# Performance work log

Measured on AMD Instinct MI355X. Metric: run time of the kernel, lower is better.

The kernel has to match this reference:

```python
import jax, jax.numpy as jnp
import numpy as np

K = 20
EPS = 1e-5


def _knn(x, k):
    # x: [B, C, N] -> indices of k nearest points, [B, N, k]
    sq = jnp.sum(x * x, axis=1)  # [B, N]
    neg_d2 = 2.0 * jnp.einsum('bcn,bcm->bnm', x, x) - sq[:, None, :] - sq[:, :, None]
    return jax.lax.top_k(neg_d2, k)[1]


def _graph_feature(x, idx):
    # x: [B, C, N], idx: [B, N, k] -> edge features [B, 2C, N, k]
    xT = x.transpose(0, 2, 1)  # [B, N, C]
    nbr = jax.vmap(lambda t, i: t[i])(xT, idx)  # [B, N, k, C]
    ctr = jnp.broadcast_to(xT[:, :, None, :], nbr.shape)
    f = jnp.concatenate([nbr - ctr, ctr], axis=-1)  # [B, N, k, 2C]
    return f.transpose(0, 3, 1, 2)


def _lrelu(x):
    return jnp.where(x > 0, x, 0.2 * x)


def _bn(x, g, b):
    # eval-mode BatchNorm with freshly-initialized running stats (mean=0, var=1)
    shp = (1, -1) + (1,) * (x.ndim - 2)
    return x * (g / jnp.sqrt(1.0 + EPS)).reshape(shp) + b.reshape(shp)


def _c2(x, w):  # 1x1 Conv2d, no bias
    return jnp.einsum('oi,bink->bonk', w, x)


def _c1(x, w):  # 1x1 Conv1d, no bias
    return jnp.einsum('oi,bin->bon', w, x)


def reference(coords, feats, w1, w2, w3, w4, w5, w6, w7, w8, w9,
              g15, b15, g6, b6, g7, b7, g8, b8):
    x0 = jnp.concatenate([coords.transpose(0, 2, 1), feats], axis=1)  # [B, 6, N]
    n = x0.shape[2]
    # EdgeConv block 1 (kNN on xyz only)
    x = _graph_feature(x0, _knn(x0[:, :3], K))  # [B, 12, N, k]
    x = _lrelu(_bn(_c2(x, w1), g15[0], b15[0]))
    x = _lrelu(_bn(_c2(x, w2), g15[1], b15[1]))
    x1 = jnp.max(x, axis=-1)  # [B, 64, N]
    # EdgeConv block 2 (dynamic kNN in feature space)
    x = _graph_feature(x1, _knn(x1, K))
    x = _lrelu(_bn(_c2(x, w3), g15[2], b15[2]))
    x = _lrelu(_bn(_c2(x, w4), g15[3], b15[3]))
    x2 = jnp.max(x, axis=-1)
    # EdgeConv block 3
    x = _graph_feature(x2, _knn(x2, K))
    x3 = jnp.max(_lrelu(_bn(_c2(x, w5), g15[4], b15[4])), axis=-1)
    # global embedding + per-point head
    xc = jnp.concatenate([x1, x2, x3], axis=1)  # [B, 192, N]
    x = _lrelu(_bn(_c1(xc, w6), g6, b6))  # [B, 1024, N]
    gmax = jnp.max(x, axis=-1, keepdims=True)
    x = jnp.concatenate([jnp.broadcast_to(gmax, (x.shape[0], x.shape[1], n)), x1, x2, x3], axis=1)  # [B,1216,N]
    x = _lrelu(_bn(_c1(x, w7), g7, b7))
    x = _lrelu(_bn(_c1(x, w8), g8, b8))
    # dropout is identity in eval mode
    x = _c1(x, w9)  # [B, 20, N]
    return x.transpose(0, 2, 1).reshape(-1, w9.shape[0])


def setup_inputs() -> dict:
    key = jax.random.key(0)
    ks = jax.random.split(key, 16)
    B, N, C = 8, 4096, 3
    s = 0.1
    return {
        'coords': jax.random.uniform(ks[0], (B, N, 3), jnp.float32),
        'feats': jax.random.normal(ks[1], (B, C, N), jnp.float32),
        'w1': s * jax.random.normal(ks[2], (64, 12), jnp.float32),
        'w2': s * jax.random.normal(ks[3], (64, 64), jnp.float32),
        'w3': s * jax.random.normal(ks[4], (64, 128), jnp.float32),
        'w4': s * jax.random.normal(ks[5], (64, 64), jnp.float32),
        'w5': s * jax.random.normal(ks[6], (64, 128), jnp.float32),
        'w6': s * jax.random.normal(ks[7], (1024, 192), jnp.float32),
        'w7': s * jax.random.normal(ks[8], (512, 1216), jnp.float32),
        'w8': s * jax.random.normal(ks[9], (256, 512), jnp.float32),
        'w9': s * jax.random.normal(ks[10], (20, 256), jnp.float32),
        'g15': jnp.ones((5, 64), jnp.float32),
        'b15': jnp.zeros((5, 64), jnp.float32),
        'g6': jnp.ones((1024,), jnp.float32),
        'b6': jnp.zeros((1024,), jnp.float32),
        'g7': jnp.ones((512,), jnp.float32),
        'b7': jnp.zeros((512,), jnp.float32),
        'g8': jnp.ones((256,), jnp.float32),
        'b8': jnp.zeros((256,), jnp.float32),
    }
```

## Files before the change

### kernel.cpp

```cpp
#include <hip/hip_runtime.h>
#include <math.h>

#define BB 8
#define NN 4096
#define KNN 20
#define EPSBN 1e-5f

__device__ __forceinline__ float lrelu(float x){ return x > 0.f ? x : 0.2f*x; }
__device__ __forceinline__ unsigned encf(float f){
  unsigned u = __float_as_uint(f);
  return (u & 0x80000000u) ? ~u : (u | 0x80000000u);
}
__device__ __forceinline__ float decf(unsigned u){
  return (u & 0x80000000u) ? __uint_as_float(u & 0x7fffffffu) : __uint_as_float(~u);
}
__device__ __forceinline__ float rdlane(float v, int l){
  return __uint_as_float(__builtin_amdgcn_readlane(__float_as_uint(v), l));
}

__global__ void prep_w(float* __restrict__ dst, const float* __restrict__ src,
                       int O, int I, int ld, int coff, const float* __restrict__ g){
  int tot = O*I;
  for(int t = blockIdx.x*blockDim.x + threadIdx.x; t < tot; t += gridDim.x*blockDim.x){
    int o = t % O, i = t / O;
    float s = g ? g[o] * (1.0f/sqrtf(1.0f+EPSBN)) : 1.0f;
    dst[(size_t)i*O + o] = src[(size_t)o*ld + coff + i] * s;
  }
}

__global__ void init_gmax(unsigned* __restrict__ g){
  int t = blockIdx.x*blockDim.x + threadIdx.x;
  if(t < BB*1024) g[t] = 0u;
}

__global__ void build_x0(const float* __restrict__ coords, const float* __restrict__ feats,
                         float* __restrict__ x0p){
  int p = blockIdx.x*blockDim.x + threadIdx.x;
  if(p >= BB*NN) return;
  int b = p / NN, n = p % NN;
  x0p[(size_t)p*6+0] = coords[(size_t)p*3+0];
  x0p[(size_t)p*6+1] = coords[(size_t)p*3+1];
  x0p[(size_t)p*6+2] = coords[(size_t)p*3+2];
  #pragma unroll
  for(int cc=0; cc<3; ++cc) x0p[(size_t)p*6+3+cc] = feats[((size_t)b*3+cc)*NN + n];
}

template<int D, int LD>
__global__ __launch_bounds__(256,3) void knn_kernel(const float* __restrict__ X, int coloff,
                                                    int* __restrict__ idxOut){
  constexpr int IG = 4;
  __shared__ float stage[2][IG][256];
  __shared__ float xi_s[IG][(D+3)&~3];
  __shared__ float sqi_s[IG];
  const int t = threadIdx.x;
  const int w = t >> 6, l = t & 63;
  const int b = blockIdx.x / (NN/IG);
  const int i0 = (blockIdx.x % (NN/IG)) * IG;
  const float* Xb = X + (size_t)b*NN*LD + coloff;

  for(int u = t; u < IG*D; u += 256) xi_s[u/D][u%D] = Xb[(size_t)(i0 + u/D)*LD + (u%D)];
  __syncthreads();
  if(t < IG){
    float s = 0.f;
    for(int d=0; d<D; ++d){ float v = xi_s[t][d]; s = fmaf(v, v, s); }
    sqi_s[t] = s;
  }
  __syncthreads();

  float v1=-INFINITY, v2=-INFINITY, v3=-INFINITY;
  int   j1=0x7fffffff, j2=0x7fffffff, j3=0x7fffffff;

  auto ins = [&](float v, int jj){
    bool b1 = v > v1, b2 = v > v2, b3 = v > v3;
    v3 = b3 ? (b2 ? v2 : v) : v3;
    j3 = b3 ? (b2 ? j2 : jj) : j3;
    v2 = b2 ? (b1 ? v1 : v) : v2;
    j2 = b2 ? (b1 ? j1 : jj) : j2;
    v1 = b1 ? v : v1;
    j1 = b1 ? jj : j1;
  };

  for(int s = 0; s < NN/256; ++s){
    const int j = s*256 + t;
    const float* row = Xb + (size_t)j*LD;
    float dot0=0.f,dot1=0.f,dot2=0.f,dot3=0.f,sqj=0.f;
    if constexpr (D % 4 == 0){
      #pragma unroll
      for(int d0=0; d0<D; d0+=4){
        const float4 v = *reinterpret_cast<const float4*>(row + d0);
        sqj = fmaf(v.x,v.x,sqj); sqj = fmaf(v.y,v.y,sqj);
        sqj = fmaf(v.z,v.z,sqj); sqj = fmaf(v.w,v.w,sqj);
        const float4 w0 = *reinterpret_cast<const float4*>(&xi_s[0][d0]);
        const float4 w1 = *reinterpret_cast<const float4*>(&xi_s[1][d0]);
        const float4 w2 = *reinterpret_cast<const float4*>(&xi_s[2][d0]);
        const float4 w3 = *reinterpret_cast<const float4*>(&xi_s[3][d0]);
        dot0 = fmaf(v.x,w0.x,dot0); dot0 = fmaf(v.y,w0.y,dot0);
        dot0 = fmaf(v.z,w0.z,dot0); dot0 = fmaf(v.w,w0.w,dot0);
        dot1 = fmaf(v.x,w1.x,dot1); dot1 = fmaf(v.y,w1.y,dot1);
        dot1 = fmaf(v.z,w1.z,dot1); dot1 = fmaf(v.w,w1.w,dot1);
        dot2 = fmaf(v.x,w2.x,dot2); dot2 = fmaf(v.y,w2.y,dot2);
        dot2 = fmaf(v.z,w2.z,dot2); dot2 = fmaf(v.w,w2.w,dot2);
        dot3 = fmaf(v.x,w3.x,dot3); dot3 = fmaf(v.y,w3.y,dot3);
        dot3 = fmaf(v.z,w3.z,dot3); dot3 = fmaf(v.w,w3.w,dot3);
      }
    } else {
      #pragma unroll
      for(int d0=0; d0<D; ++d0){
        float v = row[d0];
        sqj = fmaf(v,v,sqj);
        dot0 = fmaf(v, xi_s[0][d0], dot0); dot1 = fmaf(v, xi_s[1][d0], dot1);
        dot2 = fmaf(v, xi_s[2][d0], dot2); dot3 = fmaf(v, xi_s[3][d0], dot3);
      }
    }
    const int buf = s & 1;
    stage[buf][0][t] = 2.f*dot0 - sqj - sqi_s[0];
    stage[buf][1][t] = 2.f*dot1 - sqj - sqi_s[1];
    stage[buf][2][t] = 2.f*dot2 - sqj - sqi_s[2];
    stage[buf][3][t] = 2.f*dot3 - sqj - sqi_s[3];
    __syncthreads();
    const float4 dvv = *reinterpret_cast<const float4*>(&stage[buf][w][4*l]);
    const int jj = s*256 + 4*l;
    ins(dvv.x, jj+0); ins(dvv.y, jj+1); ins(dvv.z, jj+2); ins(dvv.w, jj+3);
  }

  int* outRow = idxOut + (size_t)(b*NN + i0 + w)*KNN;
  const float sqi = sqi_s[w];
  #pragma unroll 1
  for(int r=0;r<KNN;++r){
    float bv = v1; int bj = j1;
    #pragma unroll
    for(int off = 1; off < 64; off <<= 1){
      float ov = __shfl_xor(bv, off, 64);
      int oj = __shfl_xor(bj, off, 64);
      bool better = (ov > bv) || (ov == bv && oj < bj);
      bv = better ? ov : bv;
      bj = better ? oj : bj;
    }
    if(l == 0) outRow[r] = bj;
    if(((bj >> 2) & 63) == l){
      const float ve = v1; const int je = j1;
      v1=v2; j1=j2; v2=v3; j2=j3; v3=-INFINITY; j3=0x7fffffff;
      if(j1 == 0x7fffffff){
        #pragma unroll 1
        for(int s2=0; s2<16; ++s2){
          #pragma unroll
          for(int q=0; q<4; ++q){
            const int jj = s2*256 + 4*l + q;
            const float* rowp = Xb + (size_t)jj*LD;
            float dot=0.f, sqj=0.f;
            if constexpr (D % 4 == 0){
              #pragma unroll 4
              for(int d0=0; d0<D; d0+=4){
                const float4 v = *reinterpret_cast<const float4*>(rowp + d0);
                sqj = fmaf(v.x,v.x,sqj); sqj = fmaf(v.y,v.y,sqj);
                sqj = fmaf(v.z,v.z,sqj); sqj = fmaf(v.w,v.w,sqj);
                const float4 xw = *reinterpret_cast<const float4*>(&xi_s[w][d0]);
                dot = fmaf(v.x,xw.x,dot); dot = fmaf(v.y,xw.y,dot);
                dot = fmaf(v.z,xw.z,dot); dot = fmaf(v.w,xw.w,dot);
              }
            } else {
              #pragma unroll
              for(int d0=0; d0<D; ++d0){
                float v = rowp[d0];
                sqj = fmaf(v,v,sqj);
                dot = fmaf(v, xi_s[w][d0], dot);
              }
            }
            const float dq = 2.f*dot - sqj - sqi;
            const bool ok = (dq < ve) || (dq == ve && jj > je);
            if(ok) ins(dq, jj);
          }
        }
      }
    }
  }
}

template<int DIN, int NL>
__global__ __launch_bounds__(64,3) void edgeconv_k(
    const float* __restrict__ xin, int ldin, int cin_off,
    const int* __restrict__ idx,
    const float* __restrict__ WaT, const float* __restrict__ ba,
    const float* __restrict__ WbT, const float* __restrict__ bb,
    float* __restrict__ xout, int ldout, int cout_off){
  constexpr int PPB = 4;
  const int c = threadIdx.x;
  float wa[DIN];
  #pragma unroll
  for(int d=0; d<DIN; ++d) wa[d] = WaT[d*64 + c];
  float wb[(NL==2)?64:1];
  if constexpr (NL==2){
    #pragma unroll
    for(int d=0; d<64; ++d) wb[d] = WbT[d*64 + c];
  }
  const float bac = ba[c];
  const float bbc = (NL==2) ? bb[c] : 0.f;

  for(int pp=0; pp<PPB; ++pp){
    const int p = blockIdx.x*PPB + pp;
    const int b = p / NN;
    float ctr = (c < DIN) ? xin[(size_t)p*ldin + cin_off + c] : 0.f;
    float bacc[4] = {};
    #pragma unroll
    for(int d=0; d<DIN; ++d)
      bacc[d&3] += rdlane(ctr, d) * (WaT[(DIN+d)*64 + c] - wa[d]);
    const float base = bacc[0]+bacc[1]+bacc[2]+bacc[3];

    const int* irow = idx + (size_t)p*KNN;
    int myidx = (c < KNN) ? irow[c] : 0;
    float vmax = -INFINITY;
    int j0 = __builtin_amdgcn_readlane(myidx, 0);
    float nbr = (c < DIN) ? xin[(size_t)(b*NN + j0)*ldin + cin_off + c] : 0.f;
    for(int k=0; k<KNN; ++k){
      float nbrn = 0.f;
      if(k+1 < KNN){
        int jn = __builtin_amdgcn_readlane(myidx, k+1);
        nbrn = (c < DIN) ? xin[(size_t)(b*NN + jn)*ldin + cin_off + c] : 0.f;
      }
      float hacc[4] = {};
      #pragma unroll
      for(int d=0; d<DIN; ++d) hacc[d&3] += rdlane(nbr, d) * wa[d];
      float a1 = lrelu(base + hacc[0]+hacc[1]+hacc[2]+hacc[3] + bac);
      if constexpr (NL==2){
        float g[4] = {};
        #pragma unroll
        for(int d=0; d<64; ++d) g[d&3] += rdlane(a1, d) * wb[d];
        vmax = fmaxf(vmax, lrelu(g[0]+g[1]+g[2]+g[3] + bbc));
      } else {
        vmax = fmaxf(vmax, a1);
      }
      nbr = nbrn;
    }
    xout[(size_t)p*ldout + cout_off + c] = vmax;
  }
}

template<int EPI>
__global__ __launch_bounds__(256) void gemm_k(
    const float* __restrict__ A, int lda,
    const float* __restrict__ Bm, int Nw, int Ksz,
    const float* __restrict__ bias_n, const float* __restrict__ bias_bn,
    float* __restrict__ C, int ldc, unsigned* __restrict__ gmaxE){
  constexpr int ST = 68;
  __shared__ float At[32*ST];
  __shared__ float Bt[32*ST];
  const int t = threadIdx.x;
  const int m0 = blockIdx.x * 64;
  const int n0 = blockIdx.y * 64;
  const int tm = t >> 4, tn = t & 15;
  float acc[4][4] = {};
  for(int k0 = 0; k0 < Ksz; k0 += 32){
    #pragma unroll
    for(int r=0;r<2;++r){
      int lin = r*256 + t;
      int m = lin >> 3, f4 = lin & 7;
      float4 v = *reinterpret_cast<const float4*>(A + (size_t)(m0+m)*lda + k0 + f4*4);
      At[(f4*4+0)*ST + m] = v.x; At[(f4*4+1)*ST + m] = v.y;
      At[(f4*4+2)*ST + m] = v.z; At[(f4*4+3)*ST + m] = v.w;
    }
    #pragma unroll
    for(int r=0;r<2;++r){
      int lin = r*256 + t;
      int kk = lin >> 4, n4 = lin & 15;
      float4 v = *reinterpret_cast<const float4*>(Bm + (size_t)(k0+kk)*Nw + n0 + n4*4);
      *reinterpret_cast<float4*>(&Bt[kk*ST + n4*4]) = v;
    }
    __syncthreads();
    #pragma unroll
    for(int kk=0; kk<32; ++kk){
      float4 a4 = *reinterpret_cast<const float4*>(&At[kk*ST + tm*4]);
      float4 b4 = *reinterpret_cast<const float4*>(&Bt[kk*ST + tn*4]);
      float av[4] = {a4.x,a4.y,a4.z,a4.w};
      float bw[4] = {b4.x,b4.y,b4.z,b4.w};
      #pragma unroll
      for(int i2=0;i2<4;++i2)
        #pragma unroll
        for(int q=0;q<4;++q) acc[i2][q] += av[i2]*bw[q];
    }
    __syncthreads();
  }
  const int b = m0 / NN;
  if constexpr (EPI == 0){
    float* colm = At;
    #pragma unroll
    for(int q=0;q<4;++q){
      int n = n0 + tn*4 + q;
      float bn = bias_n[n];
      float mx = -INFINITY;
      #pragma unroll
      for(int r2=0;r2<4;++r2) mx = fmaxf(mx, lrelu(acc[r2][q] + bn));
      colm[tm*64 + tn*4 + q] = mx;
    }
    __syncthreads();
    if(t < 64){
      float mx = -INFINITY;
      #pragma unroll
      for(int r2=0;r2<16;++r2) mx = fmaxf(mx, colm[r2*64 + t]);
      atomicMax(gmaxE + b*1024 + n0 + t, encf(mx));
    }
  } else {
    #pragma unroll
    for(int r2=0;r2<4;++r2){
      int row = m0 + tm*4 + r2;
      float4 vo;
      float vv[4];
      #pragma unroll
      for(int q=0;q<4;++q){
        int n = n0 + tn*4 + q;
        float v = acc[r2][q];
        if constexpr (EPI == 1) v += bias_bn[b*512 + n] + bias_n[n];
        else v += bias_n[n];
        vv[q] = lrelu(v);
      }
      vo.x=vv[0]; vo.y=vv[1]; vo.z=vv[2]; vo.w=vv[3];
      *reinterpret_cast<float4*>(C + (size_t)row*ldc + n0 + tn*4) = vo;
    }
  }
}

__global__ __launch_bounds__(256) void bias7_kernel(const unsigned* __restrict__ gmaxE,
    const float* __restrict__ w7, const float* __restrict__ g7, float* __restrict__ b7p){
  __shared__ float gm[1024];
  const int t = threadIdx.x;
  const int b = blockIdx.x, half = blockIdx.y;
  for(int u=t; u<1024; u+=256) gm[u] = decf(gmaxE[b*1024+u]);
  __syncthreads();
  const int o = half*256 + t;
  const float* row = w7 + (size_t)o*1216;
  float acc = 0.f;
  for(int d0=0; d0<1024; d0+=4){
    float4 v = *reinterpret_cast<const float4*>(row + d0);
    acc += v.x*gm[d0] + v.y*gm[d0+1] + v.z*gm[d0+2] + v.w*gm[d0+3];
  }
  b7p[b*512+o] = acc * (g7[o] * (1.0f/sqrtf(1.0f+EPSBN)));
}

__global__ __launch_bounds__(64) void conv9_kernel(const float* __restrict__ y8,
    const float* __restrict__ w9, float* __restrict__ out){
  const int p = blockIdx.x*64 + threadIdx.x;
  float acc[20] = {};
  const float* row = y8 + (size_t)p*256;
  for(int d0=0; d0<256; d0+=4){
    float4 v = *reinterpret_cast<const float4*>(row + d0);
    #pragma unroll
    for(int o=0;o<20;++o){
      float4 w = *reinterpret_cast<const float4*>(w9 + o*256 + d0);
      acc[o] += v.x*w.x + v.y*w.y + v.z*w.z + v.w*w.w;
    }
  }
  #pragma unroll
  for(int o=0;o<20;++o) out[(size_t)p*20+o] = acc[o];
}

extern "C" void kernel_launch(void* const* d_in, const int* in_sizes, int n_in,
                              void* d_out, int out_size, void* d_ws, size_t ws_size,
                              hipStream_t stream){
  const float* coords = (const float*)d_in[0];
  const float* feats  = (const float*)d_in[1];
  const float* w1 = (const float*)d_in[2];
  const float* w2 = (const float*)d_in[3];
  const float* w3 = (const float*)d_in[4];
  const float* w4 = (const float*)d_in[5];
  const float* w5 = (const float*)d_in[6];
  const float* w6 = (const float*)d_in[7];
  const float* w7 = (const float*)d_in[8];
  const float* w8 = (const float*)d_in[9];
  const float* w9 = (const float*)d_in[10];
  const float* g15 = (const float*)d_in[11];
  const float* b15 = (const float*)d_in[12];
  const float* g6 = (const float*)d_in[13];
  const float* b6 = (const float*)d_in[14];
  const float* g7 = (const float*)d_in[15];
  const float* b7 = (const float*)d_in[16];
  const float* g8 = (const float*)d_in[17];
  const float* b8 = (const float*)d_in[18];
  float* out = (float*)d_out;
  float* ws = (float*)d_ws;

  size_t off = 0;
  float* xc   = ws + off; off += (size_t)BB*NN*192;
  float* x0p  = ws + off; off += (size_t)BB*NN*6;
  int*   idx  = (int*)(ws + off); off += (size_t)BB*NN*KNN;
  unsigned* gmaxE = (unsigned*)(ws + off); off += BB*1024;
  float* b7p  = ws + off; off += BB*512;
  float* w1t  = ws + off; off += 12*64;
  float* w2t  = ws + off; off += 64*64;
  float* w3t  = ws + off; off += 128*64;
  float* w4t  = ws + off; off += 64*64;
  float* w5t  = ws + off; off += 128*64;
  float* w6t  = ws + off; off += (size_t)192*1024;
  float* w7lt = ws + off; off += (size_t)192*512;
  float* w8t  = ws + off; off += (size_t)512*256;
  float* y7   = ws + off; off += (size_t)BB*NN*512;
  float* y8   = ws + off; off += (size_t)BB*NN*256;

  auto gb = [](int n){ return dim3((unsigned)((n + 255)/256)); };

  prep_w<<<gb(64*12),  256,0,stream>>>(w1t, w1, 64, 12, 12, 0, g15 + 0);
  prep_w<<<gb(64*64),  256,0,stream>>>(w2t, w2, 64, 64, 64, 0, g15 + 64);
  prep_w<<<gb(64*128), 256,0,stream>>>(w3t, w3, 64, 128, 128, 0, g15 + 128);
  prep_w<<<gb(64*64),  256,0,stream>>>(w4t, w4, 64, 64, 64, 0, g15 + 192);
  prep_w<<<gb(64*128), 256,0,stream>>>(w5t, w5, 64, 128, 128, 0, g15 + 256);
  prep_w<<<gb(1024*192),256,0,stream>>>(w6t, w6, 1024, 192, 192, 0, g6);
  prep_w<<<gb(512*192),256,0,stream>>>(w7lt, w7, 512, 192, 1216, 1024, g7);
  prep_w<<<gb(256*512),256,0,stream>>>(w8t, w8, 256, 512, 512, 0, g8);
  init_gmax<<<gb(BB*1024),256,0,stream>>>(gmaxE);
  build_x0<<<gb(BB*NN),256,0,stream>>>(coords, feats, x0p);

  knn_kernel<3,3><<<BB*(NN/4),256,0,stream>>>(coords, 0, idx);
  edgeconv_k<6,2><<<BB*NN/4,64,0,stream>>>(x0p, 6, 0, idx, w1t, b15+0, w2t, b15+64, xc, 192, 0);
  knn_kernel<64,192><<<BB*(NN/4),256,0,stream>>>(xc, 0, idx);
  edgeconv_k<64,2><<<BB*NN/4,64,0,stream>>>(xc, 192, 0, idx, w3t, b15+128, w4t, b15+192, xc, 192, 64);
  knn_kernel<64,192><<<BB*(NN/4),256,0,stream>>>(xc, 64, idx);
  edgeconv_k<64,1><<<BB*NN/4,64,0,stream>>>(xc, 192, 64, idx, w5t, b15+256, nullptr, nullptr, xc, 192, 128);

  gemm_k<0><<<dim3(BB*NN/64, 1024/64),256,0,stream>>>(xc, 192, w6t, 1024, 192, b6, nullptr, nullptr, 0, gmaxE);
  bias7_kernel<<<dim3(BB,2),256,0,stream>>>(gmaxE, w7, g7, b7p);
  gemm_k<1><<<dim3(BB*NN/64, 512/64),256,0,stream>>>(xc, 192, w7lt, 512, 192, b7, b7p, y7, 512, nullptr);
  gemm_k<2><<<dim3(BB*NN/64, 256/64),256,0,stream>>>(y7, 512, w8t, 256, 512, b8, nullptr, y8, 256, nullptr);
  conv9_kernel<<<BB*NN/64,64,0,stream>>>(y8, w9, out);
}
```

Baseline: 4.070 ms.

## Process four candidate rows per thread in kNN distance loop to amortize syncs

```diff
diff --git a/kernel.cpp b/kernel.cpp
--- a/kernel.cpp
+++ b/kernel.cpp
@@ -16,6 +16,10 @@
 }
 __device__ __forceinline__ float rdlane(float v, int l){
   return __uint_as_float(__builtin_amdgcn_readlane(__float_as_uint(v), l));
+}
+__device__ __forceinline__ float finalD(float dotv, float sqjv, float sqiv){
+  float ns = -sqjv - sqiv;
+  return fmaf(2.f, dotv, ns);
 }
 
 __global__ void prep_w(float* __restrict__ dst, const float* __restrict__ src,
@@ -49,7 +53,7 @@
 __global__ __launch_bounds__(256,3) void knn_kernel(const float* __restrict__ X, int coloff,
                                                     int* __restrict__ idxOut){
   constexpr int IG = 4;
-  __shared__ float stage[2][IG][256];
+  __shared__ float stage[IG][1024];
   __shared__ float xi_s[IG][(D+3)&~3];
   __shared__ float sqi_s[IG];
   const int t = threadIdx.x;
@@ -69,7 +73,6 @@
 
   float v1=-INFINITY, v2=-INFINITY, v3=-INFINITY;
   int   j1=0x7fffffff, j2=0x7fffffff, j3=0x7fffffff;
-
   auto ins = [&](float v, int jj){
     bool b1 = v > v1, b2 = v > v2, b3 = v > v3;
     v3 = b3 ? (b2 ? v2 : v) : v3;
@@ -80,47 +83,65 @@
     j1 = b1 ? jj : j1;
   };
 
-  for(int s = 0; s < NN/256; ++s){
-    const int j = s*256 + t;
-    const float* row = Xb + (size_t)j*LD;
-    float dot0=0.f,dot1=0.f,dot2=0.f,dot3=0.f,sqj=0.f;
+  #pragma unroll 1
+  for(int g=0; g<4; ++g){
+    float dot[4][4] = {{0.f,0.f,0.f,0.f},{0.f,0.f,0.f,0.f},
+                       {0.f,0.f,0.f,0.f},{0.f,0.f,0.f,0.f}};
+    float sqj[4] = {0.f,0.f,0.f,0.f};
+    const int jb = g*1024 + t;
     if constexpr (D % 4 == 0){
-      #pragma unroll
+      #pragma unroll 2
       for(int d0=0; d0<D; d0+=4){
-        const float4 v = *reinterpret_cast<const float4*>(row + d0);
-        sqj = fmaf(v.x,v.x,sqj); sqj = fmaf(v.y,v.y,sqj);
-        sqj = fmaf(v.z,v.z,sqj); sqj = fmaf(v.w,v.w,sqj);
-        const float4 w0 = *reinterpret_cast<const float4*>(&xi_s[0][d0]);
-        const float4 w1 = *reinterpret_cast<const float4*>(&xi_s[1][d0]);
-        const float4 w2 = *reinterpret_cast<const float4*>(&xi_s[2][d0]);
-        const float4 w3 = *reinterpret_cast<const float4*>(&xi_s[3][d0]);
-        dot0 = fmaf(v.x,w0.x,dot0); dot0 = fmaf(v.y,w0.y,dot0);
-        dot0 = fmaf(v.z,w0.z,dot0); dot0 = fmaf(v.w,w0.w,dot0);
-        dot1 = fmaf(v.x,w1.x,dot1); dot1 = fmaf(v.y,w1.y,dot1);
-        dot1 = fmaf(v.z,w1.z,dot1); dot1 = fmaf(v.w,w1.w,dot1);
-        dot2 = fmaf(v.x,w2.x,dot2); dot2 = fmaf(v.y,w2.y,dot2);
-        dot2 = fmaf(v.z,w2.z,dot2); dot2 = fmaf(v.w,w2.w,dot2);
-        dot3 = fmaf(v.x,w3.x,dot3); dot3 = fmaf(v.y,w3.y,dot3);
-        dot3 = fmaf(v.z,w3.z,dot3); dot3 = fmaf(v.w,w3.w,dot3);
+        float4 rv[4];
+        #pragma unroll
+        for(int k=0;k<4;++k)
+          rv[k] = *reinterpret_cast<const float4*>(Xb + (size_t)(jb + 256*k)*LD + d0);
+        float4 xw[4];
+        #pragma unroll
+        for(int q=0;q<4;++q) xw[q] = *reinterpret_cast<const float4*>(&xi_s[q][d0]);
+        #pragma unroll
+        for(int k=0;k<4;++k){
+          sqj[k] = fmaf(rv[k].x,rv[k].x,sqj[k]); sqj[k] = fmaf(rv[k].y,rv[k].y,sqj[k]);
+          sqj[k] = fmaf(rv[k].z,rv[k].z,sqj[k]); sqj[k] = fmaf(rv[k].w,rv[k].w,sqj[k]);
+          #pragma unroll
+          for(int q=0;q<4;++q){
+            dot[k][q] = fmaf(rv[k].x, xw[q].x, dot[k][q]);
+            dot[k][q] = fmaf(rv[k].y, xw[q].y, dot[k][q]);
+            dot[k][q] = fmaf(rv[k].z, xw[q].z, dot[k][q]);
+            dot[k][q] = fmaf(rv[k].w, xw[q].w, dot[k][q]);
+          }
+        }
       }
     } else {
       #pragma unroll
       for(int d0=0; d0<D; ++d0){
-        float v = row[d0];
-        sqj = fmaf(v,v,sqj);
-        dot0 = fmaf(v, xi_s[0][d0], dot0); dot1 = fmaf(v, xi_s[1][d0], dot1);
-        dot2 = fmaf(v, xi_s[2][d0], dot2); dot3 = fmaf(v, xi_s[3][d0], dot3);
-      }
-    }
-    const int buf = s & 1;
-    stage[buf][0][t] = 2.f*dot0 - sqj - sqi_s[0];
-    stage[buf][1][t] = 2.f*dot1 - sqj - sqi_s[1];
-    stage[buf][2][t] = 2.f*dot2 - sqj - sqi_s[2];
-    stage[buf][3][t] = 2.f*dot3 - sqj - sqi_s[3];
+        float rv[4];
+        #pragma unroll
+        for(int k=0;k<4;++k) rv[k] = Xb[(size_t)(jb + 256*k)*LD + d0];
+        float xw[4];
+        #pragma unroll
+        for(int q=0;q<4;++q) xw[q] = xi_s[q][d0];
+        #pragma unroll
+        for(int k=0;k<4;++k){
+          sqj[k] = fmaf(rv[k],rv[k],sqj[k]);
+          #pragma unroll
+          for(int q=0;q<4;++q) dot[k][q] = fmaf(rv[k], xw[q], dot[k][q]);
+        }
+      }
+    }
     __syncthreads();
-    const float4 dvv = *reinterpret_cast<const float4*>(&stage[buf][w][4*l]);
-    const int jj = s*256 + 4*l;
-    ins(dvv.x, jj+0); ins(dvv.y, jj+1); ins(dvv.z, jj+2); ins(dvv.w, jj+3);
+    #pragma unroll
+    for(int k=0;k<4;++k)
+      #pragma unroll
+      for(int q=0;q<4;++q)
+        stage[q][t + 256*k] = finalD(dot[k][q], sqj[k], sqi_s[q]);
+    __syncthreads();
+    #pragma unroll
+    for(int k=0;k<4;++k){
+      const float4 v = *reinterpret_cast<const float4*>(&stage[w][4*l + 256*k]);
+      const int jj = g*1024 + 256*k + 4*l;
+      ins(v.x, jj+0); ins(v.y, jj+1); ins(v.z, jj+2); ins(v.w, jj+3);
+    }
   }
 
   int* outRow = idxOut + (size_t)(b*NN + i0 + w)*KNN;
@@ -142,33 +163,37 @@
       v1=v2; j1=j2; v2=v3; j2=j3; v3=-INFINITY; j3=0x7fffffff;
       if(j1 == 0x7fffffff){
         #pragma unroll 1
-        for(int s2=0; s2<16; ++s2){
-          #pragma unroll
-          for(int q=0; q<4; ++q){
-            const int jj = s2*256 + 4*l + q;
-            const float* rowp = Xb + (size_t)jj*LD;
-            float dot=0.f, sqj=0.f;
-            if constexpr (D % 4 == 0){
-              #pragma unroll 4
-              for(int d0=0; d0<D; d0+=4){
-                const float4 v = *reinterpret_cast<const float4*>(rowp + d0);
-                sqj = fmaf(v.x,v.x,sqj); sqj = fmaf(v.y,v.y,sqj);
-                sqj = fmaf(v.z,v.z,sqj); sqj = fmaf(v.w,v.w,sqj);
-                const float4 xw = *reinterpret_cast<const float4*>(&xi_s[w][d0]);
-                dot = fmaf(v.x,xw.x,dot); dot = fmaf(v.y,xw.y,dot);
-                dot = fmaf(v.z,xw.z,dot); dot = fmaf(v.w,xw.w,dot);
+        for(int g2=0; g2<4; ++g2){
+          #pragma unroll 1
+          for(int k2=0; k2<4; ++k2){
+            const int jb2 = g2*1024 + 256*k2 + 4*l;
+            #pragma unroll 1
+            for(int e=0; e<4; ++e){
+              const int jj = jb2 + e;
+              const float* rp = Xb + (size_t)jj*LD;
+              float dotv=0.f, sq=0.f;
+              if constexpr (D % 4 == 0){
+                #pragma unroll 1
+                for(int d0=0; d0<D; d0+=4){
+                  const float4 v = *reinterpret_cast<const float4*>(rp + d0);
+                  sq = fmaf(v.x,v.x,sq); sq = fmaf(v.y,v.y,sq);
+                  sq = fmaf(v.z,v.z,sq); sq = fmaf(v.w,v.w,sq);
+                  const float4 xw = *reinterpret_cast<const float4*>(&xi_s[w][d0]);
+                  dotv = fmaf(v.x,xw.x,dotv); dotv = fmaf(v.y,xw.y,dotv);
+                  dotv = fmaf(v.z,xw.z,dotv); dotv = fmaf(v.w,xw.w,dotv);
+                }
+              } else {
+                #pragma unroll
+                for(int d0=0; d0<D; ++d0){
+                  float v = rp[d0];
+                  sq = fmaf(v,v,sq);
+                  dotv = fmaf(v, xi_s[w][d0], dotv);
+                }
               }
-            } else {
-              #pragma unroll
-              for(int d0=0; d0<D; ++d0){
-                float v = rowp[d0];
-                sqj = fmaf(v,v,sqj);
-                dot = fmaf(v, xi_s[w][d0], dot);
-              }
+              const float dq = finalD(dotv, sq, sqi);
+              const bool ok = (dq < ve) || (dq == ve && jj > je);
+              if(ok) ins(dq, jj);
             }
-            const float dq = 2.f*dot - sqj - sqi;
-            const bool ok = (dq < ve) || (dq == ve && jj > je);
-            if(ok) ins(dq, jj);
           }
         }
       }
```

Measured after the change: 5.800 ms. +42.5%, slower.
